# Performance work log

Hardware: AMD Instinct MI355X
Metric: run time of the kernel (lower is better)

## Reference

```python
import jax, jax.numpy as jnp
import numpy as np


def setup_inputs() -> dict:
    key = jax.random.key(0)
    # [B, C=3, T, H, W] raw video clips
    batch_x = jax.random.normal(key, (16, 3, 600, 72, 72), dtype=jnp.float32)
    return {"batch_x": batch_x}


def reference(batch_x):
    # Spatial mean over H, W -> RGB traces  [B, 3, N]
    x = jnp.mean(batch_x, axis=(3, 4))
    # First left singular vector of each 3xN trace matrix.
    # torch.svd(X) reduced -> U is [3, 3]; batched over B here.
    U, _, _ = jnp.linalg.svd(x, full_matrices=False)  # U: [B, 3, 3]
    S = U[..., 0]  # [B, 3] dominant left singular vector
    # Orthogonal projection P = I - S S^T (sign of S is irrelevant)
    P = jnp.eye(3, dtype=x.dtype) - jnp.einsum('bi,bj->bij', S, S)  # [B, 3, 3]
    Y = jnp.einsum('bij,bjn->bin', P, x)  # [B, 3, N]
    # Original takes channel index 1 (green) of projected signal
    return Y[:, 1, :]  # [B, N]
```

## Files before the change

kernel.cpp:

```cpp
#include <hip/hip_runtime.h>
#include <math.h>

#define HW_ELEMS 5184
#define HW_VEC   1296
#define NT       600
#define NC       3
#define NB       16
#define NSLABS   (NB * NC * NT)

__global__ __launch_bounds__(256) void mean_kernel(const float* __restrict__ in,
                                                   float* __restrict__ xbar) {
    const int bi = blockIdx.x;
    const float4* p = (const float4*)(in + (size_t)bi * HW_ELEMS);

    float s = 0.f;
    for (int i = threadIdx.x; i < HW_VEC; i += 256) {
        float4 v = p[i];
        s += (v.x + v.y) + (v.z + v.w);
    }
    #pragma unroll
    for (int off = 32; off > 0; off >>= 1)
        s += __shfl_down(s, off, 64);

    __shared__ float wsum[4];
    const int lane = threadIdx.x & 63;
    const int wid  = threadIdx.x >> 6;
    if (lane == 0) wsum[wid] = s;
    __syncthreads();
    if (threadIdx.x == 0) {
        float t = (wsum[0] + wsum[1]) + (wsum[2] + wsum[3]);
        xbar[bi] = t * (1.0f / (float)HW_ELEMS);
    }
}

__global__ __launch_bounds__(256) void project_kernel(const float* __restrict__ xbar,
                                                      float* __restrict__ out) {
    const int b = blockIdx.x;
    __shared__ float  sx[NC][NT];
    __shared__ double red[6][256];
    __shared__ float  S[3];

    const float* xb = xbar + b * (NC * NT);
    for (int i = threadIdx.x; i < NC * NT; i += 256)
        ((float*)sx)[i] = xb[i];
    __syncthreads();

    double g0 = 0, g1 = 0, g2 = 0, g3 = 0, g4 = 0, g5 = 0;
    for (int t = threadIdx.x; t < NT; t += 256) {
        double x0 = (double)sx[0][t];
        double x1 = (double)sx[1][t];
        double x2 = (double)sx[2][t];
        g0 += x0 * x0; g1 += x0 * x1; g2 += x0 * x2;
        g3 += x1 * x1; g4 += x1 * x2; g5 += x2 * x2;
    }
    red[0][threadIdx.x] = g0; red[1][threadIdx.x] = g1; red[2][threadIdx.x] = g2;
    red[3][threadIdx.x] = g3; red[4][threadIdx.x] = g4; red[5][threadIdx.x] = g5;
    __syncthreads();
    for (int s = 128; s > 0; s >>= 1) {
        if (threadIdx.x < s) {
            #pragma unroll
            for (int k = 0; k < 6; k++)
                red[k][threadIdx.x] += red[k][threadIdx.x + s];
        }
        __syncthreads();
    }

    if (threadIdx.x == 0) {
        double M[3][3] = {{red[0][0], red[1][0], red[2][0]},
                          {red[1][0], red[3][0], red[4][0]},
                          {red[2][0], red[4][0], red[5][0]}};
        for (int it = 0; it < 40; it++) {
            double tr = M[0][0] + M[1][1] + M[2][2];
            double inv = (tr > 0.0) ? (1.0 / tr) : 1.0;
            double T[3][3];
            #pragma unroll
            for (int i = 0; i < 3; i++)
                #pragma unroll
                for (int j = 0; j < 3; j++) T[i][j] = M[i][j] * inv;
            #pragma unroll
            for (int i = 0; i < 3; i++)
                #pragma unroll
                for (int j = 0; j < 3; j++) {
                    double acc = 0.0;
                    #pragma unroll
                    for (int k = 0; k < 3; k++) acc += T[i][k] * T[k][j];
                    M[i][j] = acc;
                }
        }
        int jm = 0;
        if (M[1][1] > M[jm][jm]) jm = 1;
        if (M[2][2] > M[jm][jm]) jm = 2;
        double v0 = M[0][jm], v1 = M[1][jm], v2 = M[2][jm];
        double nrm = sqrt(v0 * v0 + v1 * v1 + v2 * v2);
        double inv = (nrm > 0.0) ? (1.0 / nrm) : 0.0;
        S[0] = (float)(v0 * inv);
        S[1] = (float)(v1 * inv);
        S[2] = (float)(v2 * inv);
    }
    __syncthreads();

    const float s0 = S[0], s1 = S[1], s2 = S[2];
    for (int t = threadIdx.x; t < NT; t += 256) {
        float x0 = sx[0][t], x1 = sx[1][t], x2 = sx[2][t];
        float d = s0 * x0 + s1 * x1 + s2 * x2;
        out[b * NT + t] = x1 - s1 * d;
    }
}

extern "C" void kernel_launch(void* const* d_in, const int* in_sizes, int n_in,
                              void* d_out, int out_size, void* d_ws, size_t ws_size,
                              hipStream_t stream) {
    const float* batch_x = (const float*)d_in[0];
    float* out  = (float*)d_out;
    float* xbar = (float*)d_ws;

    mean_kernel<<<NSLABS, 256, 0, stream>>>(batch_x, xbar);
    project_kernel<<<NB, 256, 0, stream>>>(xbar, out);
}
```

Baseline: 745.4 us.

## Map one wavefront per slab with grid-stride persistent mean kernel

The mean reduction now assigns each 5184-element slab to a single 64-lane wavefront and uses a fixed grid of 2048 blocks that strides over all slabs. Loads are fully unrolled into two independent accumulators, and the block-level shared-memory reduction and barrier are dropped in favour of a wave-level xor shuffle. The aim is to remove per-block launch and sync overhead across 28,800 tiny blocks and to raise memory-level parallelism. In exchange, each wave keeps fewer loads in flight per slab than a whole block did, and the fixed grid may leave slight tail imbalance.

```diff
diff --git a/kernel.cpp b/kernel.cpp
--- a/kernel.cpp
+++ b/kernel.cpp
@@ -7,29 +7,37 @@
 #define NC       3
 #define NB       16
 #define NSLABS   (NB * NC * NT)
+#define MEAN_GRID 2048
 
 __global__ __launch_bounds__(256) void mean_kernel(const float* __restrict__ in,
                                                    float* __restrict__ xbar) {
-    const int bi = blockIdx.x;
-    const float4* p = (const float4*)(in + (size_t)bi * HW_ELEMS);
+    const int lane   = threadIdx.x & 63;
+    const int gwave  = (blockIdx.x * 256 + threadIdx.x) >> 6;
+    const int nwaves = (MEAN_GRID * 256) >> 6;
 
-    float s = 0.f;
-    for (int i = threadIdx.x; i < HW_VEC; i += 256) {
-        float4 v = p[i];
-        s += (v.x + v.y) + (v.z + v.w);
-    }
-    #pragma unroll
-    for (int off = 32; off > 0; off >>= 1)
-        s += __shfl_down(s, off, 64);
+    for (int slab = gwave; slab < NSLABS; slab += nwaves) {
+        const float4* __restrict__ p =
+            (const float4*)(in + (size_t)slab * HW_ELEMS);
 
-    __shared__ float wsum[4];
-    const int lane = threadIdx.x & 63;
-    const int wid  = threadIdx.x >> 6;
-    if (lane == 0) wsum[wid] = s;
-    __syncthreads();
-    if (threadIdx.x == 0) {
-        float t = (wsum[0] + wsum[1]) + (wsum[2] + wsum[3]);
-        xbar[bi] = t * (1.0f / (float)HW_ELEMS);
+        float s0 = 0.f, s1 = 0.f;
+        #pragma unroll
+        for (int i = 0; i < 20; i += 2) {
+            float4 a = p[(i << 6) + lane];
+            float4 b = p[((i + 1) << 6) + lane];
+            s0 += (a.x + a.y) + (a.z + a.w);
+            s1 += (b.x + b.y) + (b.z + b.w);
+        }
+        if (lane < 16) {
+            float4 v = p[1280 + lane];
+            s0 += (v.x + v.y) + (v.z + v.w);
+        }
+        float s = s0 + s1;
+
+        #pragma unroll
+        for (int off = 32; off; off >>= 1)
+            s += __shfl_xor(s, off, 64);
+
+        if (lane == 0) xbar[slab] = s * (1.0f / (float)HW_ELEMS);
     }
 }
 
@@ -114,6 +122,6 @@
     float* out  = (float*)d_out;
     float* xbar = (float*)d_ws;
 
-    mean_kernel<<<NSLABS, 256, 0, stream>>>(batch_x, xbar);
+    mean_kernel<<<MEAN_GRID, 256, 0, stream>>>(batch_x, xbar);
     project_kernel<<<NB, 256, 0, stream>>>(xbar, out);
 }
```

Result: no change. 752.7 us (+1.0%).
